# Optimization experiments

Hardware: AMD Instinct MI355X
Metric: run time of the kernel (lower is better)

Reference implementation:

```python
import jax, jax.numpy as jnp
import numpy as np

R = 512  # rnn_size == att_hid_size == input_encoding_size


def _forward(seq, att_feats, embed_w, W_word, b_word, W_h, b_h, W_img, b_img,
             W_ae, b_ae, W_c2a, b_c2a, W_sl, b_sl, W_se, b_se,
             W_hl, b_hl, W_he, b_he, W_al, b_al, W_a2h, b_a2h, W_log, b_log):
    B, T = seq.shape
    # att_embed: Linear(2048->512) + ReLU  (dropout = identity in eval)
    af = jax.nn.relu(att_feats @ W_ae + b_ae)            # [B,196,R]
    p_att = af @ W_c2a + b_c2a                            # [B,196,R] precomputed attention keys
    img_gate = af.mean(axis=1) @ W_img + b_img            # [B,6R] image contribution to gates (constant over t)
    x_emb = jax.nn.relu(embed_w[seq[:, :T - 1]])          # [B,T-1,R] word embeddings
    wg_t = jnp.swapaxes(x_emb @ W_word + b_word, 0, 1)    # [T-1,B,6R]

    def step(carry, wg):
        hx, cx = carry
        gates = wg + hx @ W_h + b_h + img_gate            # [B,6R]
        sig = jax.nn.sigmoid(gates[:, :4 * R])
        i_g = sig[:, :R]
        f_g = sig[:, R:2 * R]
        o_g = sig[:, 2 * R:3 * R]
        s_g = sig[:, 3 * R:4 * R]
        cell = jnp.maximum(gates[:, 4 * R:5 * R], gates[:, 5 * R:6 * R])
        cy = jnp.tanh(f_g * cx + i_g * cell)
        sent = s_g * cy                                   # visual sentinel
        hy = o_g * cy
        # AdaAttention
        sent_lin = jax.nn.relu(sent @ W_sl + b_sl)        # [B,R]
        sent_emb = sent_lin @ W_se + b_se
        h_lin = jnp.tanh(hy @ W_hl + b_hl)
        h_emb = h_lin @ W_he + b_he
        img_all = jnp.concatenate([sent_lin[:, None, :], af], axis=1)        # [B,197,R]
        img_all_emb = jnp.concatenate([sent_emb[:, None, :], p_att], axis=1)  # [B,197,R]
        hA = jnp.tanh(img_all_emb + h_emb[:, None, :])
        alpha = jax.nn.softmax((hA @ W_al + b_al)[..., 0], axis=-1)           # [B,197]
        cHat = jnp.einsum('ba,bad->bd', alpha, img_all)
        out = jnp.tanh((cHat + h_lin) @ W_a2h + b_a2h)    # [B,R]
        logp = jax.nn.log_softmax(out @ W_log + b_log, axis=-1)  # [B,V]
        return (hy, cy), logp

    h0 = jnp.zeros((B, R), att_feats.dtype)
    _, logps = jax.lax.scan(step, (h0, h0), wg_t)
    return jnp.swapaxes(logps, 0, 1)                      # [B,T-1,V]


def setup_inputs() -> dict:
    B, T, A, FEAT, V = 64, 21, 196, 2048, 7800
    cnt = [0]
    def nk():
        cnt[0] += 1
        return jax.random.fold_in(jax.random.key(0), cnt[0])
    def p(*shape):
        return jax.random.normal(nk(), shape, jnp.float32) * 0.02
    return dict(
        seq=jax.random.randint(nk(), (B, T), 0, V),
        att_feats=jax.random.normal(nk(), (B, A, FEAT), jnp.float32),
        embed_w=p(V, R),
        W_word=p(R, 6 * R), b_word=p(6 * R),
        W_h=p(R, 6 * R), b_h=p(6 * R),
        W_img=p(R, 6 * R), b_img=p(6 * R),
        W_ae=p(FEAT, R), b_ae=p(R),
        W_c2a=p(R, R), b_c2a=p(R),
        W_sl=p(R, R), b_sl=p(R),
        W_se=p(R, R), b_se=p(R),
        W_hl=p(R, R), b_hl=p(R),
        W_he=p(R, R), b_he=p(R),
        W_al=p(R, 1), b_al=p(1),
        W_a2h=p(R, R), b_a2h=p(R),
        W_log=p(R, V), b_log=p(V),
    )


def reference(seq, att_feats, embed_w, W_word, b_word, W_h, b_h, W_img, b_img,
              W_ae, b_ae, W_c2a, b_c2a, W_sl, b_sl, W_se, b_se,
              W_hl, b_hl, W_he, b_he, W_al, b_al, W_a2h, b_a2h, W_log, b_log):
    return _forward(seq, att_feats, embed_w, W_word, b_word, W_h, b_h, W_img, b_img,
                    W_ae, b_ae, W_c2a, b_c2a, W_sl, b_sl, W_se, b_se,
                    W_hl, b_hl, W_he, b_he, W_al, b_al, W_a2h, b_a2h, W_log, b_log)
```

## Files before the change

### kernel.cpp

```cpp
#include <hip/hip_runtime.h>

using short8 = __attribute__((ext_vector_type(8))) short;
using f32x4  = __attribute__((ext_vector_type(4))) float;
typedef unsigned short u16;
typedef unsigned int u32;

__device__ __forceinline__ float b2f(u16 u){
    return __uint_as_float(((u32)u) << 16);
}
__device__ __forceinline__ u16 f2b(float f){
    u32 x = __float_as_uint(f);
    u32 r = (x + 0x7FFFu + ((x >> 16) & 1u)) >> 16;
    return (u16)r;
}
__device__ __forceinline__ float ldx(const void* p, size_t i, bool f32){
    return f32 ? ((const float*)p)[i] : b2f(((const u16*)p)[i]);
}
__device__ __forceinline__ float sigf(float x){
    return __builtin_amdgcn_rcpf(1.0f + __expf(-x));
}
__device__ __forceinline__ float tanhf_(float x){
    float e = __expf(2.0f*x);
    return 1.0f - 2.0f*__builtin_amdgcn_rcpf(e + 1.0f);
}

#define GLDS(g, l) __builtin_amdgcn_global_load_lds((const __attribute__((address_space(1))) void*)(g), \
                        (__attribute__((address_space(3))) void*)(l), 16, 0, 0)

__global__ void probe_dtype(const void* w, int* flag){
    const u16* up = (const u16*)w;
    int lane = threadIdx.x & 63;
    int cnt = 0;
    for (int i = lane; i < 256; i += 64){
        u16 u = up[2*i];
        int e = (u >> 7) & 0xFF;
        if (e >= 100 && e <= 126) cnt++;
    }
    #pragma unroll
    for (int off = 32; off; off >>= 1) cnt += __shfl_xor(cnt, off);
    if (lane == 0) *flag = (cnt >= 192) ? 0 : 1;
}

__global__ __launch_bounds__(256) void convert_att(const void* __restrict__ in, u16* __restrict__ out,
                                                   const int* __restrict__ dflag, int total8){
    bool f32 = (*dflag != 0);
    int i = blockIdx.x*256 + threadIdx.x;
    if (i >= total8) return;
    size_t e = (size_t)i*8;
    if (f32){
        const float4* p = (const float4*)((const float*)in + e);
        float4 v0 = p[0], v1 = p[1];
        u16 o[8] = { f2b(v0.x),f2b(v0.y),f2b(v0.z),f2b(v0.w),
                     f2b(v1.x),f2b(v1.y),f2b(v1.z),f2b(v1.w) };
        *(uint4*)(out + e) = *(const uint4*)o;
    } else {
        *(uint4*)(out + e) = *(const uint4*)((const u16*)in + e);
    }
}

struct TP { const void* src[8]; u16* dst[8]; };
__global__ __launch_bounds__(256) void transpose_multi(TP tp, int K, int N, int Npad,
                                                       const int* __restrict__ dflag){
    __shared__ u16 tile[32][33];
    bool f32 = (*dflag != 0);
    const void* in = tp.src[blockIdx.z];
    u16* out = tp.dst[blockIdx.z];
    int bx = blockIdx.x, by = blockIdx.y;
    int tx = threadIdx.x, ty = threadIdx.y;
    int n = bx*32 + tx;
    #pragma unroll
    for (int i = 0; i < 32; i += 8){
        int k = by*32 + ty + i;
        u16 v = 0;
        if (n < N && k < K)
            v = f32 ? f2b(((const float*)in)[(size_t)k*N + n]) : ((const u16*)in)[(size_t)k*N + n];
        tile[ty+i][tx] = v;
    }
    __syncthreads();
    int k2 = by*32 + tx;
    #pragma unroll
    for (int i = 0; i < 32; i += 8){
        int n2 = bx*32 + ty + i;
        if (n2 < Npad && k2 < K) out[(size_t)n2*K + k2] = tile[tx][ty+i];
    }
}

__global__ __launch_bounds__(256) void gather_emb(const int* __restrict__ seq, const void* __restrict__ embed,
                                                  u16* __restrict__ x_emb, const int* __restrict__ dflag){
    bool f32 = (*dflag != 0);
    int idx = blockIdx.x*256 + threadIdx.x;
    if (idx >= 1280*512) return;
    int row = idx >> 9, r = idx & 511;
    int b = row / 20, t = row % 20;
    int w = seq[b*21 + t];
    float v = ldx(embed, (size_t)w*512 + r, f32);
    x_emb[idx] = f2b(fmaxf(v, 0.f));
}

__global__ __launch_bounds__(256) void mean_af_kernel(const u16* __restrict__ af, u16* __restrict__ mean_af){
    int b = blockIdx.x, tid = threadIdx.x;
    for (int r = tid; r < 512; r += 256){
        float s = 0.f;
        for (int a = 0; a < 196; ++a) s += b2f(af[((size_t)(b*196+a))*512 + r]);
        mean_af[b*512+r] = f2b(s * (1.0f/196.0f));
    }
}

template<int TM>
__global__ __launch_bounds__(256) void gemm_tn(const u16* __restrict__ A, const u16* __restrict__ BT,
                                               int N, int K,
                                               const void* __restrict__ bias1, const void* __restrict__ bias2,
                                               const float* __restrict__ rowAdd, int rowDiv,
                                               float* __restrict__ Cf, u16* __restrict__ Cb,
                                               int act, int Nvalid, int Mvalid,
                                               const int* __restrict__ dflag, int perm){
    constexpr int MW = TM/64;
    __shared__ u16 As[TM*64];
    __shared__ u16 Bs[64*64];
    bool f32 = (*dflag != 0);
    int tid = threadIdx.x, lane = tid & 63, w = tid >> 6;
    int lr = lane & 15, kq = lane >> 4;

    int gN = gridDim.x;
    int nwg = gN * gridDim.y;
    int flat = blockIdx.y*gN + blockIdx.x;
    int q = nwg >> 3, r = nwg & 7;
    int xcd = flat & 7, pos = flat >> 3;
    int wgid = (xcd < r ? xcd*(q+1) : r*(q+1) + (xcd-r)*q) + pos;
    int bm = wgid / gN, bn = wgid % gN;
    int row0 = bm*TM, col0 = bn*64;

    f32x4 acc[MW][4];
    #pragma unroll
    for (int m=0;m<MW;++m)
        #pragma unroll
        for (int n=0;n<4;++n) acc[m][n] = (f32x4){0.f,0.f,0.f,0.f};

    for (int k0 = 0; k0 < K; k0 += 64){
        #pragma unroll
        for (int i=0;i<TM/32;++i){
            int c = i*256 + tid;
            int row = c>>3, slot = (c&7) ^ (row&7);
            GLDS((const char*)A + ((size_t)(row0+row)*K + k0)*2 + slot*16,
                 As + (size_t)(i*256 + w*64)*8);
        }
        #pragma unroll
        for (int i=0;i<2;++i){
            int c = i*256 + tid;
            int row = c>>3, slot = (c&7) ^ (row&7);
            GLDS((const char*)BT + ((size_t)(col0+row)*K + k0)*2 + slot*16,
                 Bs + (size_t)(i*256 + w*64)*8);
        }
        __syncthreads();
        short8 av[MW][2], bv[4][2];
        #pragma unroll
        for (int ks=0;ks<2;++ks){
            #pragma unroll
            for (int m=0;m<MW;++m){
                int rrow = w*(TM/4) + m*16 + lr;
                int sl = (ks*4+kq) ^ (rrow&7);
                av[m][ks] = *(const short8*)(As + rrow*64 + sl*8);
            }
            #pragma unroll
            for (int n=0;n<4;++n){
                int rrow = n*16 + lr;
                int sl = (ks*4+kq) ^ (rrow&7);
                bv[n][ks] = *(const short8*)(Bs + rrow*64 + sl*8);
            }
        }
        #pragma unroll
        for (int ks=0;ks<2;++ks)
            #pragma unroll
            for (int m=0;m<MW;++m)
                #pragma unroll
                for (int n=0;n<4;++n)
                    acc[m][n] = __builtin_amdgcn_mfma_f32_16x16x32_bf16(av[m][ks], bv[n][ks], acc[m][n], 0,0,0);
        __syncthreads();
    }

    #pragma unroll
    for (int n=0;n<4;++n){
        int col = col0 + n*16 + lr;
        float bvv = 0.f;
        if (col < Nvalid){
            if (bias1) bvv += ldx(bias1, col, f32);
            if (bias2) bvv += ldx(bias2, col, f32);
        }
        #pragma unroll
        for (int m=0;m<MW;++m){
            #pragma unroll
            for (int rr=0;rr<4;++rr){
                int row = row0 + w*(TM/4) + m*16 + kq*4 + rr;
                if (row < Mvalid && col < Nvalid){
                    float v = acc[m][n][rr] + bvv;
                    if (rowAdd) v += rowAdd[(size_t)(row/rowDiv)*N + col];
                    if (act == 1) v = fmaxf(v, 0.f);
                    else if (act == 2) v = tanhf_(v);
                    size_t o;
                    if (perm){
                        int orow = (row % 20)*64 + row/20;
                        int ocol = (col & 511)*6 + (col >> 9);
                        o = (size_t)orow*N + ocol;
                    } else {
                        o = (size_t)row*N + col;
                    }
                    if (Cf) Cf[o] = v;
                    if (Cb) Cb[o] = f2b(v);
                }
            }
        }
    }
}

struct GP { const u16* A; const u16* BT; const void* b1; float* Cf; u16* Cb; int act; };
struct GP2 { GP g[2]; };
__global__ __launch_bounds__(256) void gemm_tn2(GP2 ps, int N, int K, int Nvalid, int Mvalid,
                                                const int* __restrict__ dflag){
    __shared__ u16 As[64*64];
    __shared__ u16 Bs[64*64];
    bool f32 = (*dflag != 0);
    GP gp = ps.g[blockIdx.z];
    int tid = threadIdx.x, lane = tid & 63, w = tid >> 6;
    int lr = lane & 15, kq = lane >> 4;

    int gN = gridDim.x;
    int nwg = gN * gridDim.y;
    int flat = blockIdx.y*gN + blockIdx.x;
    int q = nwg >> 3, r = nwg & 7;
    int xcd = flat & 7, pos = flat >> 3;
    int wgid = (xcd < r ? xcd*(q+1) : r*(q+1) + (xcd-r)*q) + pos;
    int bm = wgid / gN, bn = wgid % gN;
    int row0 = bm*64, col0 = bn*64;

    f32x4 acc[4];
    #pragma unroll
    for (int n=0;n<4;++n) acc[n] = (f32x4){0.f,0.f,0.f,0.f};

    for (int k0 = 0; k0 < K; k0 += 64){
        {
            int c = tid;
            int row = c>>3, slot = (c&7) ^ (row&7);
            GLDS((const char*)gp.A + ((size_t)(row0+row)*K + k0)*2 + slot*16,
                 As + (size_t)(w*64)*8);
            c = 256 + tid;
            row = c>>3; slot = (c&7) ^ (row&7);
            GLDS((const char*)gp.A + ((size_t)(row0+row)*K + k0)*2 + slot*16,
                 As + (size_t)(256 + w*64)*8);
            c = tid;
            row = c>>3; slot = (c&7) ^ (row&7);
            GLDS((const char*)gp.BT + ((size_t)(col0+row)*K + k0)*2 + slot*16,
                 Bs + (size_t)(w*64)*8);
            c = 256 + tid;
            row = c>>3; slot = (c&7) ^ (row&7);
            GLDS((const char*)gp.BT + ((size_t)(col0+row)*K + k0)*2 + slot*16,
                 Bs + (size_t)(256 + w*64)*8);
        }
        __syncthreads();
        short8 av[2], bv[4][2];
        #pragma unroll
        for (int ks=0;ks<2;++ks){
            int rrow = w*16 + lr;
            int sl = (ks*4+kq) ^ (rrow&7);
            av[ks] = *(const short8*)(As + rrow*64 + sl*8);
            #pragma unroll
            for (int n=0;n<4;++n){
                int rr2 = n*16 + lr;
                int sl2 = (ks*4+kq) ^ (rr2&7);
                bv[n][ks] = *(const short8*)(Bs + rr2*64 + sl2*8);
            }
        }
        #pragma unroll
        for (int ks=0;ks<2;++ks)
            #pragma unroll
            for (int n=0;n<4;++n)
                acc[n] = __builtin_amdgcn_mfma_f32_16x16x32_bf16(av[ks], bv[n][ks], acc[n], 0,0,0);
        __syncthreads();
    }

    #pragma unroll
    for (int n=0;n<4;++n){
        int col = col0 + n*16 + lr;
        float bvv = (col < Nvalid && gp.b1) ? ldx(gp.b1, col, f32) : 0.f;
        #pragma unroll
        for (int rr=0;rr<4;++rr){
            int row = row0 + w*16 + kq*4 + rr;
            if (row < Mvalid && col < Nvalid){
                float v = acc[n][rr] + bvv;
                if (gp.act == 1) v = fmaxf(v, 0.f);
                else if (gp.act == 2) v = tanhf_(v);
                size_t o = (size_t)row*N + col;
                if (gp.Cf) gp.Cf[o] = v;
                if (gp.Cb) gp.Cb[o] = f2b(v);
            }
        }
    }
}

#define GP3 52
__global__ __launch_bounds__(192) void lstm_step(const u16* __restrict__ h_in, const u16* __restrict__ WT_h,
                                                 const float* __restrict__ wgb, float* __restrict__ cstate,
                                                 u16* __restrict__ h_out, u16* __restrict__ sent_all,
                                                 u16* __restrict__ hy_all, int t){
    __shared__ float gates[16*GP3];
    int tid = threadIdx.x, lane = tid & 63, w = tid >> 6;
    int mg = blockIdx.x >> 6, rg = blockIdx.x & 63;
    int b0 = mg*16, r0 = rg*8;
    int lr = lane & 15, kq = lane >> 4, kg = kq*8;
    int c = w*16 + lr;
    int gate = c >> 3, rcol = r0 + (c & 7);
    const u16* Ap = h_in + (size_t)(b0 + lr)*512 + kg;
    const u16* Bp = WT_h + ((size_t)gate*512 + rcol)*512 + kg;
    f32x4 acc = (f32x4){0.f,0.f,0.f,0.f};
    #pragma unroll
    for (int k0 = 0; k0 < 512; k0 += 32){
        short8 a  = *(const short8*)(Ap + k0);
        short8 bf = *(const short8*)(Bp + k0);
        acc = __builtin_amdgcn_mfma_f32_16x16x32_bf16(a, bf, acc, 0,0,0);
    }
    #pragma unroll
    for (int rr = 0; rr < 4; ++rr)
        gates[(kq*4+rr)*GP3 + c] = acc[rr];
    __syncthreads();
    if (tid < 128){
        int ri = tid >> 3, rr = tid & 7;
        int b = b0 + ri, r = r0 + rr;
        const float* wp = wgb + (((size_t)t*64 + b)*512 + r)*6;
        float2 w01 = *(const float2*)(wp);
        float2 w23 = *(const float2*)(wp + 2);
        float2 w45 = *(const float2*)(wp + 4);
        float g0 = gates[ri*GP3 +      rr] + w01.x;
        float g1 = gates[ri*GP3 +  8 + rr] + w01.y;
        float g2 = gates[ri*GP3 + 16 + rr] + w23.x;
        float g3 = gates[ri*GP3 + 24 + rr] + w23.y;
        float g4 = gates[ri*GP3 + 32 + rr] + w45.x;
        float g5 = gates[ri*GP3 + 40 + rr] + w45.y;
        float ig = sigf(g0), fg = sigf(g1), og = sigf(g2), sg = sigf(g3);
        float cell = fmaxf(g4, g5);
        float co = cstate[b*512 + r];
        float cy = tanhf_(fg*co + ig*cell);
        cstate[b*512 + r] = cy;
        float sent = sg*cy, hy = og*cy;
        h_out[(size_t)b*512 + r] = f2b(hy);
        size_t rgl = (size_t)b*20 + t;
        sent_all[rgl*512 + r] = f2b(sent);
        hy_all[rgl*512 + r]   = f2b(hy);
    }
}

__global__ __launch_bounds__(256) void attn_kernel(const u16* __restrict__ sembb, const float* __restrict__ h_emb,
                                                   const float* __restrict__ sent_lin_f, const float* __restrict__ h_lin_f,
                                                   const u16* __restrict__ p_att, const u16* __restrict__ af,
                                                   const void* __restrict__ W_al, const void* __restrict__ b_al,
                                                   u16* __restrict__ ctx_in, const int* __restrict__ dflag){
    __shared__ float he_s[512];
    __shared__ float wal_s[512];
    __shared__ float se_s[512];
    __shared__ float ev[208];
    __shared__ float red2[2];
    bool f32 = (*dflag != 0);
    int flat = blockIdx.x;
    int row = (flat & 7)*160 + (flat >> 3);
    int b = row / 20;
    int tid = threadIdx.x, lane = tid & 63, w = tid >> 6;
    for (int d = tid; d < 512; d += 256){
        int ad = ((d & 7) >> 1)*128 + (d >> 3)*2 + (d & 1);
        he_s[ad]  = h_emb[(size_t)row*512 + d];
        wal_s[ad] = ldx(W_al, d, f32);
        se_s[ad]  = b2f(sembb[(size_t)row*512 + d]);
    }
    __syncthreads();
    float bal = ldx(b_al, 0, f32);

    if (w == 0){
        float p0 = 0.f;
        #pragma unroll
        for (int jp = 0; jp < 4; ++jp){
            float2 he2 = *(const float2*)&he_s[jp*128 + lane*2];
            float2 wa2 = *(const float2*)&wal_s[jp*128 + lane*2];
            float2 se2 = *(const float2*)&se_s[jp*128 + lane*2];
            p0 += tanhf_(se2.x + he2.x) * wa2.x;
            p0 += tanhf_(se2.y + he2.y) * wa2.y;
        }
        #pragma unroll
        for (int off = 32; off; off >>= 1) p0 += __shfl_xor(p0, off);
        if (lane == 0) ev[0] = p0 + bal;
    }

    const u16* pb = p_att + (size_t)b*196*512 + lane*8;
    for (int a = 1 + w; a < 197; a += 8){
        bool has2 = (a + 4 < 197);
        const u16* r0 = pb + (size_t)(a-1)*512;
        short8 v0 = *(const short8*)r0;
        short8 v1 = has2 ? *(const short8*)(r0 + (size_t)4*512) : v0;
        const u32* pk0 = (const u32*)&v0;
        const u32* pk1 = (const u32*)&v1;
        float p0 = 0.f, p1 = 0.f;
        #pragma unroll
        for (int jp = 0; jp < 4; ++jp){
            float2 he2 = *(const float2*)&he_s[jp*128 + lane*2];
            float2 wa2 = *(const float2*)&wal_s[jp*128 + lane*2];
            u32 u0 = pk0[jp], u1 = pk1[jp];
            float x00 = __uint_as_float(u0 << 16)          + he2.x;
            float x01 = __uint_as_float(u0 & 0xFFFF0000u)  + he2.y;
            float x10 = __uint_as_float(u1 << 16)          + he2.x;
            float x11 = __uint_as_float(u1 & 0xFFFF0000u)  + he2.y;
            p0 += tanhf_(x00)*wa2.x;
            p0 += tanhf_(x01)*wa2.y;
            p1 += tanhf_(x10)*wa2.x;
            p1 += tanhf_(x11)*wa2.y;
        }
        #pragma unroll
        for (int off = 32; off; off >>= 1){
            p0 += __shfl_xor(p0, off);
            p1 += __shfl_xor(p1, off);
        }
        if (lane == 0){
            ev[a] = p0 + bal;
            if (has2) ev[a+4] = p1 + bal;
        }
    }
    __syncthreads();

    if (w == 0){
        float m = -1e30f;
        for (int a = lane; a < 197; a += 64) m = fmaxf(m, ev[a]);
        #pragma unroll
        for (int off = 32; off; off >>= 1) m = fmaxf(m, __shfl_xor(m, off));
        float s = 0.f;
        for (int a = lane; a < 197; a += 64) s += __expf(ev[a] - m);
        #pragma unroll
        for (int off = 32; off; off >>= 1) s += __shfl_xor(s, off);
        if (lane == 0){ red2[0] = m; red2[1] = __builtin_amdgcn_rcpf(s); }
    }
    __syncthreads();
    float m = red2[0], inv = red2[1];
    for (int a = tid; a < 197; a += 256) ev[a] = __expf(ev[a] - m) * inv;
    __syncthreads();

    int d = tid*2;
    const u16* afb = af + (size_t)b*196*512 + d;
    float s0 = 0.f, s1 = 0.f, t0 = 0.f, t1 = 0.f;
    for (int a = 0; a < 196; a += 2){
        float e0 = ev[a+1], e1 = ev[a+2];
        u32 u0 = *(const u32*)(afb + (size_t)a*512);
        u32 u1 = *(const u32*)(afb + (size_t)(a+1)*512);
        s0 += e0 * __uint_as_float(u0 << 16);
        s1 += e0 * __uint_as_float(u0 & 0xFFFF0000u);
        t0 += e1 * __uint_as_float(u1 << 16);
        t1 += e1 * __uint_as_float(u1 & 0xFFFF0000u);
    }
    float e00 = ev[0];
    float a0 = e00*sent_lin_f[(size_t)row*512 + d]     + s0 + t0 + h_lin_f[(size_t)row*512 + d];
    float a1 = e00*sent_lin_f[(size_t)row*512 + d + 1] + s1 + t1 + h_lin_f[(size_t)row*512 + d + 1];
    ctx_in[(size_t)row*512 + d]     = f2b(a0);
    ctx_in[(size_t)row*512 + d + 1] = f2b(a1);
}

__global__ __launch_bounds__(256) void logsoftmax_kernel(const u16* __restrict__ logits, void* __restrict__ out,
                                                         const int* __restrict__ dflag){
    __shared__ float red[256];
    bool f32 = (*dflag != 0);
    int row = blockIdx.x, tid = threadIdx.x;
    const u16* lp = logits + (size_t)row*7808;
    float m = -1e30f;
    for (int v = tid; v < 7800; v += 256) m = fmaxf(m, b2f(lp[v]));
    red[tid] = m; __syncthreads();
    for (int s = 128; s; s >>= 1){ if (tid < s) red[tid] = fmaxf(red[tid], red[tid+s]); __syncthreads(); }
    m = red[0]; __syncthreads();
    float s = 0.f;
    for (int v = tid; v < 7800; v += 256) s += __expf(b2f(lp[v]) - m);
    red[tid] = s; __syncthreads();
    for (int st = 128; st; st >>= 1){ if (tid < st) red[tid] += red[tid+st]; __syncthreads(); }
    float lse = m + __logf(red[0]);
    if (f32){
        float* op = (float*)out + (size_t)row*7800;
        for (int v = tid; v < 7800; v += 256) op[v] = b2f(lp[v]) - lse;
    } else {
        u16* op = (u16*)out + (size_t)row*7800;
        for (int v = tid; v < 7800; v += 256) op[v] = f2b(b2f(lp[v]) - lse);
    }
}

extern "C" void kernel_launch(void* const* d_in, const int* in_sizes, int n_in,
                              void* d_out, int out_size, void* d_ws, size_t ws_size,
                              hipStream_t stream){
    (void)in_sizes; (void)n_in; (void)out_size; (void)ws_size;
    const int* seq    = (const int*)d_in[0];
    const void* att   = d_in[1];
    const void* embed = d_in[2];
    const void* W_word= d_in[3];  const void* b_word = d_in[4];
    const void* W_h   = d_in[5];  const void* b_h    = d_in[6];
    const void* W_img = d_in[7];  const void* b_img  = d_in[8];
    const void* W_ae  = d_in[9];  const void* b_ae   = d_in[10];
    const void* W_c2a = d_in[11]; const void* b_c2a  = d_in[12];
    const void* W_sl  = d_in[13]; const void* b_sl   = d_in[14];
    const void* W_se  = d_in[15]; const void* b_se   = d_in[16];
    const void* W_hl  = d_in[17]; const void* b_hl   = d_in[18];
    const void* W_he  = d_in[19]; const void* b_he   = d_in[20];
    const void* W_al  = d_in[21]; const void* b_al   = d_in[22];
    const void* W_a2h = d_in[23]; const void* b_a2h  = d_in[24];
    const void* W_log = d_in[25]; const void* b_log  = d_in[26];

    char* p = (char*)d_ws;
    auto alloc = [&](size_t bytes)->char*{ char* r = p; p += (bytes + 255) & ~(size_t)255; return r; };

    int* dflag   = (int*)alloc(256);
    u16* WT_ae   = (u16*)alloc((size_t)512*2048*2);
    u16* WT_word = (u16*)alloc((size_t)3072*512*2);
    u16* WT_h    = (u16*)alloc((size_t)3072*512*2);
    u16* WT_img  = (u16*)alloc((size_t)3072*512*2);
    u16* WT_c2a  = (u16*)alloc((size_t)512*512*2);
    u16* WT_sl   = (u16*)alloc((size_t)512*512*2);
    u16* WT_se   = (u16*)alloc((size_t)512*512*2);
    u16* WT_hl   = (u16*)alloc((size_t)512*512*2);
    u16* WT_he   = (u16*)alloc((size_t)512*512*2);
    u16* WT_a2h  = (u16*)alloc((size_t)512*512*2);
    u16* WT_log  = (u16*)alloc((size_t)7808*512*2);
    u16* af      = (u16*)alloc((size_t)12544*512*2);
    u16* p_att   = (u16*)alloc((size_t)12544*512*2);
    u16* meanb   = (u16*)alloc((size_t)64*512*2);
    float* imgg  = (float*)alloc((size_t)64*3072*4);
    u16* xemb    = (u16*)alloc((size_t)1280*512*2);
    float* wgb   = (float*)alloc((size_t)1280*3072*4);
    u16* hb0     = (u16*)alloc((size_t)64*512*2);
    u16* hb1     = (u16*)alloc((size_t)64*512*2);
    float* cst   = (float*)alloc((size_t)64*512*4);
    u16* sent_all= (u16*)alloc((size_t)1280*512*2);
    u16* hy_all  = (u16*)alloc((size_t)1280*512*2);
    float* slf   = (float*)alloc((size_t)1280*512*4);
    u16* slb     = (u16*)alloc((size_t)1280*512*2);
    float* hlf   = (float*)alloc((size_t)1280*512*4);
    u16* hlb     = (u16*)alloc((size_t)1280*512*2);
    u16* sembb   = (u16*)alloc((size_t)1280*512*2);
    float* hemb  = (float*)alloc((size_t)1280*512*4);
    u16* ctx     = (u16*)alloc((size_t)1280*512*2);
    u16* a2hb    = (u16*)alloc((size_t)1280*512*2);
    u16* logits  = (u16*)alloc((size_t)1280*7808*2);

    u16* attb = (u16*)wgb;

    probe_dtype<<<1, 64, 0, stream>>>(W_ae, dflag);

    dim3 tb(32,8);
    {
        TP t6{};
        t6.src[0]=W_c2a; t6.dst[0]=WT_c2a;
        t6.src[1]=W_sl;  t6.dst[1]=WT_sl;
        t6.src[2]=W_se;  t6.dst[2]=WT_se;
        t6.src[3]=W_hl;  t6.dst[3]=WT_hl;
        t6.src[4]=W_he;  t6.dst[4]=WT_he;
        t6.src[5]=W_a2h; t6.dst[5]=WT_a2h;
        transpose_multi<<<dim3(16,16,6), tb, 0, stream>>>(t6, 512, 512, 512, dflag);
        TP t3{};
        t3.src[0]=W_word; t3.dst[0]=WT_word;
        t3.src[1]=W_h;    t3.dst[1]=WT_h;
        t3.src[2]=W_img;  t3.dst[2]=WT_img;
        transpose_multi<<<dim3(96,16,3), tb, 0, stream>>>(t3, 512, 3072, 3072, dflag);
        TP ta{}; ta.src[0]=W_ae; ta.dst[0]=WT_ae;
        transpose_multi<<<dim3(16,64,1), tb, 0, stream>>>(ta, 2048, 512, 512, dflag);
        TP tl{}; tl.src[0]=W_log; tl.dst[0]=WT_log;
        transpose_multi<<<dim3(244,16,1), tb, 0, stream>>>(tl, 512, 7800, 7808, dflag);
    }

    convert_att<<<12544, 256, 0, stream>>>(att, attb, dflag, 12544*2048/8);

    gemm_tn<128><<<dim3(8,98), 256, 0, stream>>>(attb, WT_ae, 512, 2048,
                                                 b_ae, nullptr, nullptr, 1, nullptr, af, 1, 512, 12544, dflag, 0);
    gemm_tn<128><<<dim3(8,98), 256, 0, stream>>>(af, WT_c2a, 512, 512,
                                                 b_c2a, nullptr, nullptr, 1, nullptr, p_att, 0, 512, 12544, dflag, 0);
    mean_af_kernel<<<64, 256, 0, stream>>>(af, meanb);
    gemm_tn<64><<<dim3(48,1), 256, 0, stream>>>(meanb, WT_img, 3072, 512,
                                                b_img, nullptr, nullptr, 1, imgg, nullptr, 0, 3072, 64, dflag, 0);
    gather_emb<<<2560, 256, 0, stream>>>(seq, embed, xemb, dflag);
    gemm_tn<64><<<dim3(48,20), 256, 0, stream>>>(xemb, WT_word, 3072, 512,
                                                 b_word, b_h, imgg, 20, wgb, nullptr, 0, 3072, 1280, dflag, 1);

    hipMemsetAsync(hb0, 0, (size_t)64*512*2, stream);
    hipMemsetAsync(cst, 0, (size_t)64*512*4, stream);

    for (int t = 0; t < 20; ++t){
        const u16* hin = (t & 1) ? hb1 : hb0;
        u16* hout      = (t & 1) ? hb0 : hb1;
        lstm_step<<<256, 192, 0, stream>>>(hin, WT_h, wgb, cst, hout, sent_all, hy_all, t);
    }

    GP2 pa{};
    pa.g[0] = { sent_all, WT_sl, b_sl, slf, slb, 1 };
    pa.g[1] = { hy_all,   WT_hl, b_hl, hlf, hlb, 2 };
    gemm_tn2<<<dim3(8,20,2), 256, 0, stream>>>(pa, 512, 512, 512, 1280, dflag);
    GP2 pb{};
    pb.g[0] = { slb, WT_se, b_se, nullptr, sembb, 0 };
    pb.g[1] = { hlb, WT_he, b_he, hemb, nullptr, 0 };
    gemm_tn2<<<dim3(8,20,2), 256, 0, stream>>>(pb, 512, 512, 512, 1280, dflag);

    attn_kernel<<<1280, 256, 0, stream>>>(sembb, hemb, slf, hlf, p_att, af, W_al, b_al, ctx, dflag);
    gemm_tn<64><<<dim3(8,20), 256, 0, stream>>>(ctx, WT_a2h, 512, 512,
                                                b_a2h, nullptr, nullptr, 1, nullptr, a2hb, 2, 512, 1280, dflag, 0);
    gemm_tn<128><<<dim3(122,10), 256, 0, stream>>>(a2hb, WT_log, 7808, 512,
                                                   b_log, nullptr, nullptr, 1, nullptr, logits, 0, 7800, 1280, dflag, 0);
    logsoftmax_kernel<<<1280, 256, 0, stream>>>(logits, d_out, dflag);
}
```

Measured before the change: 423.3 us.

## Split attention into parallel score and context kernels; cache logits in registers

The fused attention kernel is split in two. The first kernel computes the 197 attention scores per row across four y-chunks, which gives four times as many blocks, and writes them to a global buffer. The second kernel then does the softmax and the weighted context sum. The log-softmax kernel also keeps each thread's logits in registers, so it no longer reloads them from global memory in the sum and write passes. The costs are one extra launch, a global round trip for the scores, and higher register pressure from the 31-element array.

```diff
diff --git a/kernel.cpp b/kernel.cpp
--- a/kernel.cpp
+++ b/kernel.cpp
@@ -347,51 +347,36 @@
     }
 }
 
-__global__ __launch_bounds__(256) void attn_kernel(const u16* __restrict__ sembb, const float* __restrict__ h_emb,
-                                                   const float* __restrict__ sent_lin_f, const float* __restrict__ h_lin_f,
-                                                   const u16* __restrict__ p_att, const u16* __restrict__ af,
-                                                   const void* __restrict__ W_al, const void* __restrict__ b_al,
-                                                   u16* __restrict__ ctx_in, const int* __restrict__ dflag){
+__global__ __launch_bounds__(256) void attn_score(const u16* __restrict__ sembb, const float* __restrict__ h_emb,
+                                                  const u16* __restrict__ p_att,
+                                                  const void* __restrict__ W_al, const void* __restrict__ b_al,
+                                                  float* __restrict__ evg, const int* __restrict__ dflag){
     __shared__ float he_s[512];
     __shared__ float wal_s[512];
-    __shared__ float se_s[512];
-    __shared__ float ev[208];
-    __shared__ float red2[2];
     bool f32 = (*dflag != 0);
     int flat = blockIdx.x;
     int row = (flat & 7)*160 + (flat >> 3);
     int b = row / 20;
+    int chunk = blockIdx.y;
     int tid = threadIdx.x, lane = tid & 63, w = tid >> 6;
     for (int d = tid; d < 512; d += 256){
         int ad = ((d & 7) >> 1)*128 + (d >> 3)*2 + (d & 1);
         he_s[ad]  = h_emb[(size_t)row*512 + d];
         wal_s[ad] = ldx(W_al, d, f32);
-        se_s[ad]  = b2f(sembb[(size_t)row*512 + d]);
     }
     __syncthreads();
     float bal = ldx(b_al, 0, f32);
-
-    if (w == 0){
-        float p0 = 0.f;
-        #pragma unroll
-        for (int jp = 0; jp < 4; ++jp){
-            float2 he2 = *(const float2*)&he_s[jp*128 + lane*2];
-            float2 wa2 = *(const float2*)&wal_s[jp*128 + lane*2];
-            float2 se2 = *(const float2*)&se_s[jp*128 + lane*2];
-            p0 += tanhf_(se2.x + he2.x) * wa2.x;
-            p0 += tanhf_(se2.y + he2.y) * wa2.y;
-        }
-        #pragma unroll
-        for (int off = 32; off; off >>= 1) p0 += __shfl_xor(p0, off);
-        if (lane == 0) ev[0] = p0 + bal;
-    }
-
-    const u16* pb = p_att + (size_t)b*196*512 + lane*8;
-    for (int a = 1 + w; a < 197; a += 8){
-        bool has2 = (a + 4 < 197);
-        const u16* r0 = pb + (size_t)(a-1)*512;
-        short8 v0 = *(const short8*)r0;
-        short8 v1 = has2 ? *(const short8*)(r0 + (size_t)4*512) : v0;
+    float* evr = evg + (size_t)row*256;
+
+    for (int j = w; chunk + 4*j < 197; j += 8){
+        int a0i = chunk + 4*j;
+        int a1i = a0i + 16;
+        bool has2 = (a1i < 197);
+        const u16* r0 = (a0i == 0) ? (sembb + (size_t)row*512)
+                                   : (p_att + ((size_t)(b*196 + a0i-1))*512);
+        const u16* r1 = has2 ? (p_att + ((size_t)(b*196 + a1i-1))*512) : r0;
+        short8 v0 = *(const short8*)(r0 + lane*8);
+        short8 v1 = *(const short8*)(r1 + lane*8);
         const u32* pk0 = (const u32*)&v0;
         const u32* pk1 = (const u32*)&v1;
         float p0 = 0.f, p1 = 0.f;
@@ -415,12 +400,25 @@
             p1 += __shfl_xor(p1, off);
         }
         if (lane == 0){
-            ev[a] = p0 + bal;
-            if (has2) ev[a+4] = p1 + bal;
-        }
-    }
+            evr[a0i] = p0 + bal;
+            if (has2) evr[a1i] = p1 + bal;
+        }
+    }
+}
+
+__global__ __launch_bounds__(256) void attn_ctx(const float* __restrict__ evg,
+                                                const float* __restrict__ sent_lin_f, const float* __restrict__ h_lin_f,
+                                                const u16* __restrict__ af,
+                                                u16* __restrict__ ctx_in){
+    __shared__ float ev[208];
+    __shared__ float red2[2];
+    int flat = blockIdx.x;
+    int row = (flat & 7)*160 + (flat >> 3);
+    int b = row / 20;
+    int tid = threadIdx.x, lane = tid & 63, w = tid >> 6;
+    const float* evr = evg + (size_t)row*256;
+    for (int a = tid; a < 197; a += 256) ev[a] = evr[a];
     __syncthreads();
-
     if (w == 0){
         float m = -1e30f;
         for (int a = lane; a < 197; a += 64) m = fmaxf(m, ev[a]);
@@ -462,22 +460,37 @@
     bool f32 = (*dflag != 0);
     int row = blockIdx.x, tid = threadIdx.x;
     const u16* lp = logits + (size_t)row*7808;
+    float xs[31];
     float m = -1e30f;
-    for (int v = tid; v < 7800; v += 256) m = fmaxf(m, b2f(lp[v]));
+    #pragma unroll
+    for (int k = 0; k < 31; ++k){
+        int v = k*256 + tid;
+        xs[k] = (v < 7800) ? b2f(lp[v]) : -1e30f;
+        m = fmaxf(m, xs[k]);
+    }
     red[tid] = m; __syncthreads();
     for (int s = 128; s; s >>= 1){ if (tid < s) red[tid] = fmaxf(red[tid], red[tid+s]); __syncthreads(); }
     m = red[0]; __syncthreads();
     float s = 0.f;
-    for (int v = tid; v < 7800; v += 256) s += __expf(b2f(lp[v]) - m);
+    #pragma unroll
+    for (int k = 0; k < 31; ++k) s += __expf(xs[k] - m);
     red[tid] = s; __syncthreads();
     for (int st = 128; st; st >>= 1){ if (tid < st) red[tid] += red[tid+st]; __syncthreads(); }
     float lse = m + __logf(red[0]);
     if (f32){
         float* op = (float*)out + (size_t)row*7800;
-        for (int v = tid; v < 7800; v += 256) op[v] = b2f(lp[v]) - lse;
+        #pragma unroll
+        for (int k = 0; k < 31; ++k){
+            int v = k*256 + tid;
+            if (v < 7800) op[v] = xs[k] - lse;
+        }
     } else {
         u16* op = (u16*)out + (size_t)row*7800;
-        for (int v = tid; v < 7800; v += 256) op[v] = f2b(b2f(lp[v]) - lse);
+        #pragma unroll
+        for (int k = 0; k < 31; ++k){
+            int v = k*256 + tid;
+            if (v < 7800) op[v] = f2b(xs[k] - lse);
+        }
     }
 }
 
@@ -535,6 +548,7 @@
     float* hemb  = (float*)alloc((size_t)1280*512*4);
     u16* ctx     = (u16*)alloc((size_t)1280*512*2);
     u16* a2hb    = (u16*)alloc((size_t)1280*512*2);
+    float* evg   = (float*)alloc((size_t)1280*256*4);
     u16* logits  = (u16*)alloc((size_t)1280*7808*2);
 
     u16* attb = (u16*)wgb;
@@ -593,7 +607,9 @@
     pb.g[1] = { hlb, WT_he, b_he, hemb, nullptr, 0 };
     gemm_tn2<<<dim3(8,20,2), 256, 0, stream>>>(pb, 512, 512, 512, 1280, dflag);
 
-    attn_kernel<<<1280, 256, 0, stream>>>(sembb, hemb, slf, hlf, p_att, af, W_al, b_al, ctx, dflag);
+    attn_score<<<dim3(1280,4), 256, 0, stream>>>(sembb, hemb, p_att, W_al, b_al, evg, dflag);
+    attn_ctx<<<1280, 256, 0, stream>>>(evg, slf, hlf, af, ctx);
+
     gemm_tn<64><<<dim3(8,20), 256, 0, stream>>>(ctx, WT_a2h, 512, 512,
                                                 b_a2h, nullptr, nullptr, 1, nullptr, a2hb, 2, 512, 1280, dflag, 0);
     gemm_tn<128><<<dim3(122,10), 256, 0, stream>>>(a2hb, WT_log, 7808, 512,
```

New measurement: 407.4 us. -3.7%, faster.
